# Optimization experiments

Measured on AMD Instinct MI355X. Metric: run time of the kernel, lower is better.

The kernel has to match this reference:

```python
import jax, jax.numpy as jnp
import numpy as np

IN_F = 1024
OUT_F = 1024
GRID_SIZE = 5
SPLINE_ORDER = 3
GRID_RANGE = (-1.0, 1.0)


def _make_grid():
    h = (GRID_RANGE[1] - GRID_RANGE[0]) / GRID_SIZE
    g = jnp.arange(-SPLINE_ORDER, GRID_SIZE + SPLINE_ORDER + 1, dtype=jnp.float32) * h + GRID_RANGE[0]
    return jnp.broadcast_to(g, (IN_F, g.shape[0]))  # (F, grid_size + 2*order + 1)


def setup_inputs() -> dict:
    key = jax.random.key(0)
    k1, k2, k3, k4 = jax.random.split(key, 4)
    B = 8192
    x = jax.random.normal(k1, (B, IN_F), dtype=jnp.float32)
    base_weight = jax.random.normal(k2, (OUT_F, IN_F), dtype=jnp.float32) / np.sqrt(IN_F)
    # mimic reset_parameters: uniform noise scaled by scale_noise/grid_size
    spline_weight = (jax.random.uniform(k3, (OUT_F, IN_F, GRID_SIZE + SPLINE_ORDER)) - 0.5) * (0.1 / GRID_SIZE)
    spline_scaler = jax.random.normal(k4, (OUT_F, IN_F), dtype=jnp.float32) / np.sqrt(IN_F)
    grid = _make_grid()
    return {"x": x, "base_weight": base_weight, "spline_weight": spline_weight,
            "spline_scaler": spline_scaler, "grid": grid}


def b_splines(x, grid):
    # x: (B, F); grid: (F, G) with G = grid_size + 2*order + 1
    xe = x[:, :, None]  # (B, F, 1)
    bases = ((xe >= grid[:, :-1]) & (xe < grid[:, 1:])).astype(x.dtype)  # (B, F, G-1)
    for k in range(1, SPLINE_ORDER + 1):
        left = (xe - grid[:, : -(k + 1)]) / (grid[:, k:-1] - grid[:, : -(k + 1)])
        right = (grid[:, k + 1 :] - xe) / (grid[:, k + 1 :] - grid[:, 1:-k])
        bases = left * bases[:, :, :-1] + right * bases[:, :, 1:]
    return bases  # (B, F, grid_size + order)


def reference(x, base_weight, spline_weight, spline_scaler, grid):
    base_out = jax.nn.silu(x) @ base_weight.T  # (B, O)
    basis = b_splines(x, grid)  # (B, F, C)
    scaled_w = spline_weight * spline_scaler[:, :, None]  # (O, F, C)
    spline_out = jnp.einsum('bfc,ofc->bo', basis, scaled_w)
    return base_out + spline_out
```

## Files before the change

### kernel.cpp

```cpp
#include <hip/hip_runtime.h>
#include <hip/hip_bf16.h>

#define IN_F   1024
#define OUT_F  1024
#define NCH    9
#define KDIM   9216
#define BATCH  8192

#define BM 256
#define BN 256
#define BK 32
#define KHALF 4608
#define NTK (KHALF / BK)
#define SLOTA 8192
#define KCH  288

typedef __attribute__((ext_vector_type(4)))  float  f32x4;
typedef __attribute__((ext_vector_type(8)))  __bf16 bf16x8;

typedef __attribute__((address_space(3))) unsigned short       lds_u16;
typedef const __attribute__((address_space(1))) unsigned short glb_u16;

__device__ inline unsigned short f2bf(float f) {
    union { float f; unsigned int u; } v; v.f = f;
    unsigned int u = v.u;
    unsigned int r = (u + 0x7FFFu + ((u >> 16) & 1u)) >> 16;
    return (unsigned short)r;
}

__global__ void prep_kernel(const float* __restrict__ x,
                            const float* __restrict__ bw,
                            const float* __restrict__ sw,
                            const float* __restrict__ sc,
                            unsigned short* __restrict__ A,
                            unsigned short* __restrict__ Wf) {
    const int bid = blockIdx.x;
    if (bid < 4096) {
        int idx = bid * 256 + threadIdx.x;
        const float4* xp = (const float4*)(x + (size_t)idx * 8);
        float4 x0 = xp[0], x1 = xp[1];
        float xs[8] = {x0.x, x0.y, x0.z, x0.w, x1.x, x1.y, x1.z, x1.w};

        unsigned short vals[8][9];
#pragma unroll
        for (int e = 0; e < 8; ++e) {
            float v  = xs[e];
            float s  = v / (1.0f + __expf(-v));
            float t  = (v + 2.2f) * 2.5f;
            float jf = floorf(t);
            int   j  = (int)jf;
            float u  = t - jf;
            float u2 = u * u, u3 = u2 * u;
            float p0 = u3 * (1.0f / 6.0f);
            float p1 = (-3.0f * u3 + 3.0f * u2 + 3.0f * u + 1.0f) * (1.0f / 6.0f);
            float p2 = (3.0f * u3 - 6.0f * u2 + 4.0f) * (1.0f / 6.0f);
            float om = 1.0f - u;
            float p3 = om * om * om * (1.0f / 6.0f);
            bool valid = (v >= -2.2f) && (v < 2.2f);
#pragma unroll
            for (int c = 0; c < 8; ++c) {
                int p = j - c;
                float bv = 0.0f;
                if (valid)
                    bv = (p == 0) ? p0 : (p == 1) ? p1 : (p == 2) ? p2 : (p == 3) ? p3 : 0.0f;
                vals[e][c] = f2bf(bv);
            }
            vals[e][8] = f2bf(s);
        }

        int r = idx >> 7, f8 = idx & 127;
        unsigned short* base = A + (size_t)r * KDIM + f8 * 8;
#pragma unroll
        for (int c = 0; c < 9; ++c) {
            uint4 pk;
            pk.x = (unsigned int)vals[0][c] | ((unsigned int)vals[1][c] << 16);
            pk.y = (unsigned int)vals[2][c] | ((unsigned int)vals[3][c] << 16);
            pk.z = (unsigned int)vals[4][c] | ((unsigned int)vals[5][c] << 16);
            pk.w = (unsigned int)vals[6][c] | ((unsigned int)vals[7][c] << 16);
            *(uint4*)(base + (size_t)c * 1024) = pk;
        }
    } else {
        int idx = (bid - 4096) * 256 + threadIdx.x;
        int o = idx >> 10, f = idx & 1023;
        float scale = sc[idx];
        const float4* swp = (const float4*)(sw + (size_t)idx * 8);
        float4 w0 = swp[0], w1 = swp[1];
        float wv[9] = {w0.x * scale, w0.y * scale, w0.z * scale, w0.w * scale,
                       w1.x * scale, w1.y * scale, w1.z * scale, w1.w * scale,
                       bw[idx]};
        const int nb   = o >> 4;
        const int lane = (o & 15) + (((f >> 3) & 3) << 4);
        const int jj   = f & 7;
        const int kcf  = f >> 5;
#pragma unroll
        for (int c = 0; c < 9; ++c) {
            size_t ui = (((size_t)nb * KCH + (c * 32 + kcf)) << 9) + lane * 8 + jj;
            Wf[ui] = f2bf(wv[c]);
        }
    }
}

#define DECLS(q) \
    const int ci##q = (q) * 512 + tid; \
    const int lo##q = ci##q << 3; \
    const int rr##q = ci##q >> 2; \
    const int cl##q = (((ci##q & 3) ^ ((rr##q >> 1) & 3)) << 3); \
    const unsigned short* srcA##q = Ap + (size_t)(m0 + rr##q) * KDIM + kbase + cl##q;

#define STAGE_A(q, ns) do { \
    __builtin_amdgcn_global_load_lds((glb_u16*)srcA##q, (lds_u16*)(ns) + lo##q, 16, 0, 0); \
    srcA##q += BK; } while (0)

#define RDA(mi) (*(const bf16x8*)&sA[(rowa + (mi) * 16) * BK + koff])

#define LDB(ni, tt) (*(const bf16x8*)&Wf[((((size_t)(nbB + (ni))) * KCH + kcb + (tt)) << 9) + lsh])

#define MM4(av, mi, B0, B1, B2, B3) \
    acc[mi][0] = __builtin_amdgcn_mfma_f32_16x16x32_bf16(av, B0, acc[mi][0], 0, 0, 0); \
    acc[mi][1] = __builtin_amdgcn_mfma_f32_16x16x32_bf16(av, B1, acc[mi][1], 0, 0, 0); \
    acc[mi][2] = __builtin_amdgcn_mfma_f32_16x16x32_bf16(av, B2, acc[mi][2], 0, 0, 0); \
    acc[mi][3] = __builtin_amdgcn_mfma_f32_16x16x32_bf16(av, B3, acc[mi][3], 0, 0, 0);

#define BODY(t, C0, C1, C2, C3, N0, N1, N2, N3) do { \
    unsigned short* ns = lds + (((t) + 3) & 3) * SLOTA; \
    if ((t) + 3 < NTK) { STAGE_A(0, ns); STAGE_A(1, ns); } \
    if ((t) + 1 < NTK) { N0 = LDB(0, (t) + 1); N1 = LDB(1, (t) + 1); \
                         N2 = LDB(2, (t) + 1); N3 = LDB(3, (t) + 1); } \
    const unsigned short* sA = lds + ((t) & 3) * SLOTA; \
    __builtin_amdgcn_s_setprio(1); \
    { bf16x8 a0 = RDA(0); MM4(a0, 0, C0, C1, C2, C3) } \
    { bf16x8 a1 = RDA(1); MM4(a1, 1, C0, C1, C2, C3) } \
    { bf16x8 a2 = RDA(2); MM4(a2, 2, C0, C1, C2, C3) } \
    { bf16x8 a3 = RDA(3); MM4(a3, 3, C0, C1, C2, C3) } \
    { bf16x8 a4 = RDA(4); MM4(a4, 4, C0, C1, C2, C3) } \
    { bf16x8 a5 = RDA(5); MM4(a5, 5, C0, C1, C2, C3) } \
    { bf16x8 a6 = RDA(6); MM4(a6, 6, C0, C1, C2, C3) } \
    { bf16x8 a7 = RDA(7); MM4(a7, 7, C0, C1, C2, C3) } \
    __builtin_amdgcn_s_setprio(0); \
    if ((t) <= NTK - 4)      asm volatile("s_waitcnt vmcnt(8)" ::: "memory"); \
    else if ((t) == NTK - 3) asm volatile("s_waitcnt vmcnt(6)" ::: "memory"); \
    else if ((t) == NTK - 2) asm volatile("s_waitcnt vmcnt(4)" ::: "memory"); \
    else                     asm volatile("s_waitcnt vmcnt(0)" ::: "memory"); \
    __builtin_amdgcn_s_barrier(); \
} while (0)

__global__ __launch_bounds__(512, 2) void gemm_bg(
    const unsigned short* __restrict__ Ap,
    const unsigned short* __restrict__ Wf,
    float* __restrict__ C, float* __restrict__ P, int mode) {
    __shared__ unsigned short lds[4 * SLOTA];

    const int tid  = threadIdx.x;
    const int wave = tid >> 6;
    const int lane = tid & 63;
    const int lm16 = lane & 15;
    const int lhi  = lane >> 4;
    const int koff = ((lhi ^ ((lm16 >> 1) & 3)) << 3);
    const int lsh  = lane << 3;

    const int bid  = blockIdx.x;
    const int mg   = bid & 3;
    const int kb   = (bid >> 2) & 1;
    const int j    = bid >> 3;
    const int m0   = (mg * 8 + (j >> 2)) * BM;
    const int n0   = (j & 3) * BN;
    const int kbase = kb * KHALF;

    const int wr = wave >> 2;
    const int wc = wave & 3;
    const int rowa = wr * 128 + lm16;
    const int nbB  = (n0 >> 4) + wc * 4;
    const int kcb  = kb * NTK;

    f32x4 acc[8][4];
#pragma unroll
    for (int i = 0; i < 8; ++i)
#pragma unroll
        for (int jn = 0; jn < 4; ++jn) acc[i][jn] = (f32x4)(0.0f);

    DECLS(0) DECLS(1)

    bf16x8 bA0, bA1, bA2, bA3, bB0, bB1, bB2, bB3;

    {
        unsigned short* ns = lds;
        STAGE_A(0, ns); STAGE_A(1, ns);
    }
    bA0 = LDB(0, 0); bA1 = LDB(1, 0); bA2 = LDB(2, 0); bA3 = LDB(3, 0);
    {
        unsigned short* ns = lds + SLOTA;
        STAGE_A(0, ns); STAGE_A(1, ns);
    }
    {
        unsigned short* ns = lds + 2 * SLOTA;
        STAGE_A(0, ns); STAGE_A(1, ns);
    }
    asm volatile("s_waitcnt vmcnt(8)" ::: "memory");
    __builtin_amdgcn_s_barrier();

#pragma unroll 2
    for (int t = 0; t < NTK; t += 2) {
        BODY(t,     bA0, bA1, bA2, bA3, bB0, bB1, bB2, bB3);
        BODY(t + 1, bB0, bB1, bB2, bB3, bA0, bA1, bA2, bA3);
    }

    const int orow = m0 + wr * 128 + (lhi << 2);
    const int ocol = n0 + wc * 64 + lm16;
    if (mode) {
#pragma unroll
        for (int mi = 0; mi < 8; ++mi)
#pragma unroll
            for (int ni = 0; ni < 4; ++ni)
#pragma unroll
                for (int r = 0; r < 4; ++r)
                    atomicAdd(&C[(size_t)(orow + mi * 16 + r) * OUT_F + (ocol + ni * 16)], acc[mi][ni][r]);
    } else {
        float* dst = kb ? P : C;
#pragma unroll
        for (int mi = 0; mi < 8; ++mi)
#pragma unroll
            for (int ni = 0; ni < 4; ++ni)
#pragma unroll
                for (int r = 0; r < 4; ++r)
                    dst[(size_t)(orow + mi * 16 + r) * OUT_F + (ocol + ni * 16)] = acc[mi][ni][r];
    }
}

__global__ void add_kernel(float* __restrict__ C, const float* __restrict__ P) {
    int i = blockIdx.x * blockDim.x + threadIdx.x;
    if (i >= BATCH * OUT_F / 4) return;
    f32x4* c4 = (f32x4*)C;
    const f32x4* p4 = (const f32x4*)P;
    c4[i] = c4[i] + p4[i];
}

extern "C" void kernel_launch(void* const* d_in, const int* in_sizes, int n_in,
                              void* d_out, int out_size, void* d_ws, size_t ws_size,
                              hipStream_t stream) {
    const float* x             = (const float*)d_in[0];
    const float* base_weight   = (const float*)d_in[1];
    const float* spline_weight = (const float*)d_in[2];
    const float* spline_scaler = (const float*)d_in[3];
    float* out = (float*)d_out;

    const size_t wbytes = (size_t)OUT_F * KDIM * 2;
    const size_t abytes = (size_t)BATCH * KDIM * 2;
    const size_t pbytes = (size_t)BATCH * OUT_F * 4;
    unsigned short* Wf   = (unsigned short*)d_ws;
    unsigned short* Abuf = (unsigned short*)((char*)d_ws + wbytes);
    float*          P    = (float*)((char*)d_ws + wbytes + abytes);

    const int mode = (ws_size >= wbytes + abytes + pbytes) ? 0 : 1;
    if (mode == 1)
        (void)hipMemsetAsync(d_out, 0, pbytes, stream);

    prep_kernel<<<8192, 256, 0, stream>>>(x, base_weight, spline_weight,
                                          spline_scaler, Abuf, Wf);

    gemm_bg<<<256, 512, 0, stream>>>(Abuf, Wf, out, P, mode);

    if (mode == 0)
        add_kernel<<<(BATCH * OUT_F / 4 + 255) / 256, 256, 0, stream>>>(out, P);
}
```

Before: 227.8 us.

## Stage both GEMM operands through LDS with BK=64 and 8-phase ping-pong schedule

Weights are now written row-major (O x KDIM) instead of the MFMA-fragment layout, and the GEMM stages both A and B tiles into LDS with async global-to-LDS loads at BK=64 and XOR swizzling. The main loop is split into eight barrier-separated phases per two K tiles, interleaving LDS fragment reads, partial prefetches of the next tiles and 16-MFMA clusters. The aim is to raise B reuse across waves and to overlap memory traffic with compute. In exchange it uses 128KB of LDS per block and adds many more barriers per K step.

Measured after the change: 195.1 us. -14.3%, faster.

```diff
diff --git a/kernel.cpp b/kernel.cpp
--- a/kernel.cpp
+++ b/kernel.cpp
@@ -9,11 +9,10 @@
 
 #define BM 256
 #define BN 256
-#define BK 32
+#define BK 64
 #define KHALF 4608
 #define NTK (KHALF / BK)
-#define SLOTA 8192
-#define KCH  288
+#define NT2 (NTK / 2)
 
 typedef __attribute__((ext_vector_type(4)))  float  f32x4;
 typedef __attribute__((ext_vector_type(8)))  __bf16 bf16x8;
@@ -33,7 +32,7 @@
                             const float* __restrict__ sw,
                             const float* __restrict__ sc,
                             unsigned short* __restrict__ A,
-                            unsigned short* __restrict__ Wf) {
+                            unsigned short* __restrict__ W) {
     const int bid = blockIdx.x;
     if (bid < 4096) {
         int idx = bid * 256 + threadIdx.x;
@@ -85,78 +84,73 @@
         float scale = sc[idx];
         const float4* swp = (const float4*)(sw + (size_t)idx * 8);
         float4 w0 = swp[0], w1 = swp[1];
-        float wv[9] = {w0.x * scale, w0.y * scale, w0.z * scale, w0.w * scale,
-                       w1.x * scale, w1.y * scale, w1.z * scale, w1.w * scale,
-                       bw[idx]};
-        const int nb   = o >> 4;
-        const int lane = (o & 15) + (((f >> 3) & 3) << 4);
-        const int jj   = f & 7;
-        const int kcf  = f >> 5;
-#pragma unroll
-        for (int c = 0; c < 9; ++c) {
-            size_t ui = (((size_t)nb * KCH + (c * 32 + kcf)) << 9) + lane * 8 + jj;
-            Wf[ui] = f2bf(wv[c]);
-        }
+        unsigned short* Wb = W + (size_t)o * KDIM + f;
+        Wb[0 * 1024] = f2bf(w0.x * scale);
+        Wb[1 * 1024] = f2bf(w0.y * scale);
+        Wb[2 * 1024] = f2bf(w0.z * scale);
+        Wb[3 * 1024] = f2bf(w0.w * scale);
+        Wb[4 * 1024] = f2bf(w1.x * scale);
+        Wb[5 * 1024] = f2bf(w1.y * scale);
+        Wb[6 * 1024] = f2bf(w1.z * scale);
+        Wb[7 * 1024] = f2bf(w1.w * scale);
+        Wb[8 * 1024] = f2bf(bw[idx]);
     }
 }
 
-#define DECLS(q) \
-    const int ci##q = (q) * 512 + tid; \
-    const int lo##q = ci##q << 3; \
-    const int rr##q = ci##q >> 2; \
-    const int cl##q = (((ci##q & 3) ^ ((rr##q >> 1) & 3)) << 3); \
-    const unsigned short* srcA##q = Ap + (size_t)(m0 + rr##q) * KDIM + kbase + cl##q;
-
-#define STAGE_A(q, ns) do { \
-    __builtin_amdgcn_global_load_lds((glb_u16*)srcA##q, (lds_u16*)(ns) + lo##q, 16, 0, 0); \
-    srcA##q += BK; } while (0)
-
-#define RDA(mi) (*(const bf16x8*)&sA[(rowa + (mi) * 16) * BK + koff])
-
-#define LDB(ni, tt) (*(const bf16x8*)&Wf[((((size_t)(nbB + (ni))) * KCH + kcb + (tt)) << 9) + lsh])
-
-#define MM4(av, mi, B0, B1, B2, B3) \
-    acc[mi][0] = __builtin_amdgcn_mfma_f32_16x16x32_bf16(av, B0, acc[mi][0], 0, 0, 0); \
-    acc[mi][1] = __builtin_amdgcn_mfma_f32_16x16x32_bf16(av, B1, acc[mi][1], 0, 0, 0); \
-    acc[mi][2] = __builtin_amdgcn_mfma_f32_16x16x32_bf16(av, B2, acc[mi][2], 0, 0, 0); \
-    acc[mi][3] = __builtin_amdgcn_mfma_f32_16x16x32_bf16(av, B3, acc[mi][3], 0, 0, 0);
-
-#define BODY(t, C0, C1, C2, C3, N0, N1, N2, N3) do { \
-    unsigned short* ns = lds + (((t) + 3) & 3) * SLOTA; \
-    if ((t) + 3 < NTK) { STAGE_A(0, ns); STAGE_A(1, ns); } \
-    if ((t) + 1 < NTK) { N0 = LDB(0, (t) + 1); N1 = LDB(1, (t) + 1); \
-                         N2 = LDB(2, (t) + 1); N3 = LDB(3, (t) + 1); } \
-    const unsigned short* sA = lds + ((t) & 3) * SLOTA; \
-    __builtin_amdgcn_s_setprio(1); \
-    { bf16x8 a0 = RDA(0); MM4(a0, 0, C0, C1, C2, C3) } \
-    { bf16x8 a1 = RDA(1); MM4(a1, 1, C0, C1, C2, C3) } \
-    { bf16x8 a2 = RDA(2); MM4(a2, 2, C0, C1, C2, C3) } \
-    { bf16x8 a3 = RDA(3); MM4(a3, 3, C0, C1, C2, C3) } \
-    { bf16x8 a4 = RDA(4); MM4(a4, 4, C0, C1, C2, C3) } \
-    { bf16x8 a5 = RDA(5); MM4(a5, 5, C0, C1, C2, C3) } \
-    { bf16x8 a6 = RDA(6); MM4(a6, 6, C0, C1, C2, C3) } \
-    { bf16x8 a7 = RDA(7); MM4(a7, 7, C0, C1, C2, C3) } \
-    __builtin_amdgcn_s_setprio(0); \
-    if ((t) <= NTK - 4)      asm volatile("s_waitcnt vmcnt(8)" ::: "memory"); \
-    else if ((t) == NTK - 3) asm volatile("s_waitcnt vmcnt(6)" ::: "memory"); \
-    else if ((t) == NTK - 2) asm volatile("s_waitcnt vmcnt(4)" ::: "memory"); \
-    else                     asm volatile("s_waitcnt vmcnt(0)" ::: "memory"); \
-    __builtin_amdgcn_s_barrier(); \
-} while (0)
-
-__global__ __launch_bounds__(512, 2) void gemm_bg(
+#define STG_A(h, tt, bsel) do { \
+    __builtin_amdgcn_global_load_lds((glb_u16*)(pa0 + (size_t)(h) * 128 * KDIM + (size_t)(tt) * 64), \
+        (lds_u16*)lds + (bsel) * 32768 + (h) * 8192 + da0, 16, 0, 0); \
+    __builtin_amdgcn_global_load_lds((glb_u16*)(pa1 + (size_t)(h) * 128 * KDIM + (size_t)(tt) * 64), \
+        (lds_u16*)lds + (bsel) * 32768 + (h) * 8192 + da1, 16, 0, 0); \
+} while (0)
+
+#define STG_B(h, tt, bsel) do { \
+    __builtin_amdgcn_global_load_lds((glb_u16*)(pb0 + (size_t)(h) * 128 * KDIM + (size_t)(tt) * 64), \
+        (lds_u16*)lds + (bsel) * 32768 + 16384 + (h) * 8192 + da0, 16, 0, 0); \
+    __builtin_amdgcn_global_load_lds((glb_u16*)(pb1 + (size_t)(h) * 128 * KDIM + (size_t)(tt) * 64), \
+        (lds_u16*)lds + (bsel) * 32768 + 16384 + (h) * 8192 + da1, 16, 0, 0); \
+} while (0)
+
+#define RD(off) (*(const bf16x8*)&lds[off])
+
+#define RDA4(ab, moff) do { \
+    _Pragma("unroll") for (int i = 0; i < 4; ++i) { \
+        a[i][0] = RD((ab) + ra + (moff) + i * 1024 + ko0); \
+        a[i][1] = RD((ab) + ra + (moff) + i * 1024 + ko1); } \
+} while (0)
+
+#define RDB2(bb, NB) do { \
+    _Pragma("unroll") for (int jq = 0; jq < 2; ++jq) { \
+        b[(NB) + jq][0] = RD((bb) + rb + ((NB) + jq) * 1024 + ko0); \
+        b[(NB) + jq][1] = RD((bb) + rb + ((NB) + jq) * 1024 + ko1); } \
+} while (0)
+
+#define MM16(MB, NB) do { \
+    _Pragma("unroll") for (int i = 0; i < 4; ++i) \
+        _Pragma("unroll") for (int jq = 0; jq < 2; ++jq) { \
+            acc[(MB) + i][(NB) + jq] = __builtin_amdgcn_mfma_f32_16x16x32_bf16( \
+                a[i][0], b[(NB) + jq][0], acc[(MB) + i][(NB) + jq], 0, 0, 0); \
+            acc[(MB) + i][(NB) + jq] = __builtin_amdgcn_mfma_f32_16x16x32_bf16( \
+                a[i][1], b[(NB) + jq][1], acc[(MB) + i][(NB) + jq], 0, 0, 0); } \
+} while (0)
+
+#define BAR()  __builtin_amdgcn_s_barrier()
+#define LGK0() asm volatile("s_waitcnt lgkmcnt(0)" ::: "memory")
+#define PRIO(n) __builtin_amdgcn_s_setprio(n)
+
+__global__ __launch_bounds__(512, 2) void gemm_8p(
     const unsigned short* __restrict__ Ap,
-    const unsigned short* __restrict__ Wf,
+    const unsigned short* __restrict__ Wp,
     float* __restrict__ C, float* __restrict__ P, int mode) {
-    __shared__ unsigned short lds[4 * SLOTA];
+    __shared__ unsigned short lds[65536];
 
     const int tid  = threadIdx.x;
     const int wave = tid >> 6;
     const int lane = tid & 63;
     const int lm16 = lane & 15;
     const int lhi  = lane >> 4;
-    const int koff = ((lhi ^ ((lm16 >> 1) & 3)) << 3);
-    const int lsh  = lane << 3;
+    const int ko0  = ((lhi ^ (lm16 & 7)) << 3);
+    const int ko1  = ko0 ^ 32;
 
     const int bid  = blockIdx.x;
     const int mg   = bid & 3;
@@ -168,9 +162,8 @@
 
     const int wr = wave >> 2;
     const int wc = wave & 3;
-    const int rowa = wr * 128 + lm16;
-    const int nbB  = (n0 >> 4) + wc * 4;
-    const int kcb  = kb * NTK;
+    const int ra = ((wr << 7) + lm16) << 6;
+    const int rb = ((wc << 6) + lm16) << 6;
 
     f32x4 acc[8][4];
 #pragma unroll
@@ -178,30 +171,60 @@
 #pragma unroll
         for (int jn = 0; jn < 4; ++jn) acc[i][jn] = (f32x4)(0.0f);
 
-    DECLS(0) DECLS(1)
-
-    bf16x8 bA0, bA1, bA2, bA3, bB0, bB1, bB2, bB3;
-
-    {
-        unsigned short* ns = lds;
-        STAGE_A(0, ns); STAGE_A(1, ns);
-    }
-    bA0 = LDB(0, 0); bA1 = LDB(1, 0); bA2 = LDB(2, 0); bA3 = LDB(3, 0);
-    {
-        unsigned short* ns = lds + SLOTA;
-        STAGE_A(0, ns); STAGE_A(1, ns);
-    }
-    {
-        unsigned short* ns = lds + 2 * SLOTA;
-        STAGE_A(0, ns); STAGE_A(1, ns);
-    }
-    asm volatile("s_waitcnt vmcnt(8)" ::: "memory");
-    __builtin_amdgcn_s_barrier();
-
-#pragma unroll 2
-    for (int t = 0; t < NTK; t += 2) {
-        BODY(t,     bA0, bA1, bA2, bA3, bB0, bB1, bB2, bB3);
-        BODY(t + 1, bB0, bB1, bB2, bB3, bA0, bA1, bA2, bA3);
+    const int ci0 = tid, ci1 = 512 + tid;
+    const int da0 = ci0 << 3, da1 = ci1 << 3;
+    const unsigned short* pa0 = Ap + (size_t)(m0 + (ci0 >> 3)) * KDIM + kbase + (((ci0 & 7) ^ ((ci0 >> 3) & 7)) << 3);
+    const unsigned short* pa1 = Ap + (size_t)(m0 + (ci1 >> 3)) * KDIM + kbase + (((ci1 & 7) ^ ((ci1 >> 3) & 7)) << 3);
+    const unsigned short* pb0 = Wp + (size_t)(n0 + (ci0 >> 3)) * KDIM + kbase + (((ci0 & 7) ^ ((ci0 >> 3) & 7)) << 3);
+    const unsigned short* pb1 = Wp + (size_t)(n0 + (ci1 >> 3)) * KDIM + kbase + (((ci1 & 7) ^ ((ci1 >> 3) & 7)) << 3);
+
+    bf16x8 a[4][2], b[4][2];
+
+    STG_B(0, 0, 0); STG_B(1, 0, 0); STG_A(0, 0, 0); STG_A(1, 0, 0);
+    STG_B(0, 1, 1); STG_B(1, 1, 1);
+    asm volatile("s_waitcnt vmcnt(4)" ::: "memory");
+    BAR();
+
+#pragma unroll 1
+    for (int t = 0; t < NT2; ++t) {
+        const int T = 2 * t;
+        const bool pf = (t < NT2 - 1);
+
+        RDA4(0, 0); RDB2(16384, 0);
+        STG_A(0, T + 1, 1);
+        BAR(); LGK0(); PRIO(1); MM16(0, 0); PRIO(0); BAR();
+
+        RDB2(16384, 2);
+        STG_A(1, T + 1, 1);
+        BAR(); LGK0(); PRIO(1); MM16(0, 2); PRIO(0); BAR();
+
+        RDA4(0, 4096);
+        if (pf) STG_B(0, T + 2, 0);
+        BAR(); LGK0(); PRIO(1); MM16(4, 2); PRIO(0); BAR();
+
+        if (pf) STG_B(1, T + 2, 0);
+        BAR(); PRIO(1); MM16(4, 0); PRIO(0);
+        if (pf) asm volatile("s_waitcnt vmcnt(4)" ::: "memory");
+        else    asm volatile("s_waitcnt vmcnt(0)" ::: "memory");
+        BAR();
+
+        RDA4(32768, 0); RDB2(49152, 0);
+        if (pf) STG_A(0, T + 2, 0);
+        BAR(); LGK0(); PRIO(1); MM16(0, 0); PRIO(0); BAR();
+
+        RDB2(49152, 2);
+        if (pf) STG_A(1, T + 2, 0);
+        BAR(); LGK0(); PRIO(1); MM16(0, 2); PRIO(0); BAR();
+
+        RDA4(32768, 4096);
+        if (pf) STG_B(0, T + 3, 1);
+        BAR(); LGK0(); PRIO(1); MM16(4, 2); PRIO(0); BAR();
+
+        if (pf) STG_B(1, T + 3, 1);
+        BAR(); PRIO(1); MM16(4, 0); PRIO(0);
+        if (pf) asm volatile("s_waitcnt vmcnt(4)" ::: "memory");
+        else    asm volatile("s_waitcnt vmcnt(0)" ::: "memory");
+        BAR();
     }
 
     const int orow = m0 + wr * 128 + (lhi << 2);
@@ -246,7 +269,7 @@
     const size_t wbytes = (size_t)OUT_F * KDIM * 2;
     const size_t abytes = (size_t)BATCH * KDIM * 2;
     const size_t pbytes = (size_t)BATCH * OUT_F * 4;
-    unsigned short* Wf   = (unsigned short*)d_ws;
+    unsigned short* Wc   = (unsigned short*)d_ws;
     unsigned short* Abuf = (unsigned short*)((char*)d_ws + wbytes);
     float*          P    = (float*)((char*)d_ws + wbytes + abytes);
 
@@ -255,9 +278,9 @@
         (void)hipMemsetAsync(d_out, 0, pbytes, stream);
 
     prep_kernel<<<8192, 256, 0, stream>>>(x, base_weight, spline_weight,
-                                          spline_scaler, Abuf, Wf);
-
-    gemm_bg<<<256, 512, 0, stream>>>(Abuf, Wf, out, P, mode);
+                                          spline_scaler, Abuf, Wc);
+
+    gemm_8p<<<256, 512, 0, stream>>>(Abuf, Wc, out, P, mode);
 
     if (mode == 0)
         add_kernel<<<(BATCH * OUT_F / 4 + 255) / 256, 256, 0, stream>>>(out, P);
```
